# Performance work log

Hardware: AMD Instinct MI355X
Metric: run time of the kernel (lower is better)

Reference implementation:

```python
import jax, jax.numpy as jnp
import numpy as np

B, S, D, H = 4, 2048, 512, 8
HD = D // H


def _xavier(key, shape):
    fan_in, fan_out = shape[1], shape[0]
    limit = float(np.sqrt(6.0 / (fan_in + fan_out)))
    return jax.random.uniform(key, shape, jnp.float32, -limit, limit)


def setup_inputs() -> dict:
    key = jax.random.key(0)
    ks = jax.random.split(key, 7)
    return {
        "query": jax.random.normal(ks[0], (B, S, D), jnp.float32),
        "key": jax.random.normal(ks[1], (B, S, D), jnp.float32),
        "value": jax.random.normal(ks[2], (B, S, D), jnp.float32),
        "Wq": _xavier(ks[3], (D, D)), "bq": jnp.zeros((D,), jnp.float32),
        "Wk": _xavier(ks[4], (D, D)), "bk": jnp.zeros((D,), jnp.float32),
        "Wv": _xavier(ks[5], (D, D)), "bv": jnp.zeros((D,), jnp.float32),
        "Wo": _xavier(ks[6], (D, D)), "bo": jnp.zeros((D,), jnp.float32),
    }


def _split_heads(x):
    # [B,S,D] -> [B,H,S,HD]
    return x.reshape(B, S, H, HD).transpose(0, 2, 1, 3)


def reference(query, key, value, Wq, bq, Wk, bk, Wv, bv, Wo, bo):
    # torch Linear: y = x @ W.T + b
    Q = _split_heads(query @ Wq.T + bq)
    K = _split_heads(key @ Wk.T + bk)
    V = _split_heads(value @ Wv.T + bv)
    scale = 1.0 / jnp.sqrt(jnp.asarray(HD, Q.dtype))
    logits = jnp.einsum("bhqd,bhkd->bhqk", Q, K) * scale  # [B,H,S,S]
    attn = jax.nn.softmax(logits, axis=-1)
    ctx = jnp.einsum("bhqk,bhkd->bhqd", attn, V)
    ctx = ctx.transpose(0, 2, 1, 3).reshape(B, S, D)
    return ctx @ Wo.T + bo
```

## Files before the change

### kernel.cpp

```cpp
#include <hip/hip_runtime.h>
#include <hip/hip_bf16.h>


#define BB 4
#define SS 2048
#define DD 512
#define HH 8
#define HDD 64

typedef __bf16 bf16;
typedef __bf16 bf16x8 __attribute__((ext_vector_type(8)));
typedef float f32x4 __attribute__((ext_vector_type(4)));
typedef float f32x16 __attribute__((ext_vector_type(16)));

__device__ __forceinline__ int swz(int row, int byteInRow) {
    return row * 128 + (byteInRow ^ ((row & 7) << 4));
}

__device__ __forceinline__ void gload16(const void* g, void* l) {
    __builtin_amdgcn_global_load_lds(
        (const __attribute__((address_space(1))) void*)g,
        (__attribute__((address_space(3))) void*)l, 16, 0, 0);
}

__global__ __launch_bounds__(256) void cvt_bf16(
    const float* __restrict__ xq, const float* __restrict__ xk, const float* __restrict__ xv,
    const float* __restrict__ wq, const float* __restrict__ wk, const float* __restrict__ wv,
    const float* __restrict__ wo,
    bf16* __restrict__ xqb, bf16* __restrict__ xkb, bf16* __restrict__ xvb,
    bf16* __restrict__ wqb, bf16* __restrict__ wkb, bf16* __restrict__ wvb,
    bf16* __restrict__ wob)
{
    const int NX = BB * SS * DD / 4;
    const int NW = DD * DD / 4;
    const int total = 3 * NX + 4 * NW;
    for (int g = blockIdx.x * 256 + threadIdx.x; g < total; g += gridDim.x * 256) {
        const float* src; bf16* dst; int off;
        if (g < 3 * NX) {
            int s = g >> 20; off = g & (NX - 1);
            src = s == 0 ? xq : s == 1 ? xk : xv;
            dst = s == 0 ? xqb : s == 1 ? xkb : xvb;
        } else {
            int gg = g - 3 * NX; int s = gg >> 16; off = gg & (NW - 1);
            src = s == 0 ? wq : s == 1 ? wk : s == 2 ? wv : wo;
            dst = s == 0 ? wqb : s == 1 ? wkb : s == 2 ? wvb : wob;
        }
        float4 v = ((const float4*)src)[off];
        union { bf16 h[4]; ushort4 u; } c;
        c.h[0] = (bf16)v.x; c.h[1] = (bf16)v.y; c.h[2] = (bf16)v.z; c.h[3] = (bf16)v.w;
        ((ushort4*)dst)[off] = c.u;
    }
}

__global__ __launch_bounds__(256) void gemm_qkv(
    const bf16* __restrict__ Xq, const bf16* __restrict__ Xk, const bf16* __restrict__ Xv,
    const bf16* __restrict__ Wq, const bf16* __restrict__ Wk, const bf16* __restrict__ Wv,
    const float* __restrict__ bq, const float* __restrict__ bk, const float* __restrict__ bv,
    bf16* __restrict__ Qb, bf16* __restrict__ Kb, bf16* __restrict__ Vt)
{
    const int lin = blockIdx.x;
    const int w = (lin & 7) * 192 + (lin >> 3);
    const int z = w / 512, rem = w & 511;
    const int m0 = (rem >> 3) * 128, n0 = (rem & 7) * 64;

    const bf16* __restrict__ A  = (z == 0) ? Xq : (z == 1) ? Xk : Xv;
    const bf16* __restrict__ Wt = (z == 0) ? Wq : (z == 1) ? Wk : Wv;
    const float* __restrict__ bias = (z == 0) ? bq : (z == 1) ? bk : bv;

    __shared__ char lds[24576];
    char* As = lds;
    char* Bs = lds + 16384;

    const int t = threadIdx.x, wid = t >> 6, lane = t & 63;
    const int lr = lane & 15, lg = lane >> 4;

    float bv4[4];
#pragma unroll
    for (int ni = 0; ni < 4; ni++) bv4[ni] = bias[n0 + ni * 16 + lr];

    const int srow = lane >> 3, s_l = (lane & 7) ^ srow;

    f32x4 acc[2][4] = {};

    for (int k0 = 0; k0 < DD; k0 += 64) {
#pragma unroll
        for (int i = 0; i < 4; i++) {
            int row = 32 * wid + 8 * i + srow;
            gload16(A + (size_t)(m0 + row) * DD + k0 + s_l * 8, As + (32 * wid + 8 * i) * 128);
        }
#pragma unroll
        for (int i = 0; i < 2; i++) {
            int row = 16 * wid + 8 * i + srow;
            gload16(Wt + (size_t)(n0 + row) * DD + k0 + s_l * 8, Bs + (16 * wid + 8 * i) * 128);
        }
        __syncthreads();
#pragma unroll
        for (int kk = 0; kk < 2; kk++) {
            bf16x8 af[2], bfr[4];
#pragma unroll
            for (int mi = 0; mi < 2; mi++)
                af[mi] = *(const bf16x8*)(As + swz(wid * 32 + mi * 16 + lr, kk * 64 + lg * 16));
#pragma unroll
            for (int ni = 0; ni < 4; ni++)
                bfr[ni] = *(const bf16x8*)(Bs + swz(ni * 16 + lr, kk * 64 + lg * 16));
#pragma unroll
            for (int mi = 0; mi < 2; mi++)
#pragma unroll
                for (int ni = 0; ni < 4; ni++)
                    acc[mi][ni] = __builtin_amdgcn_mfma_f32_16x16x32_bf16(af[mi], bfr[ni], acc[mi][ni], 0, 0, 0);
        }
        __syncthreads();
    }

#pragma unroll
    for (int mi = 0; mi < 2; mi++)
#pragma unroll
        for (int ni = 0; ni < 4; ni++) {
            int col = n0 + ni * 16 + lr;
#pragma unroll
            for (int j = 0; j < 4; j++) {
                int row = m0 + wid * 32 + mi * 16 + lg * 4 + j;
                float v = acc[mi][ni][j] + bv4[ni];
                if (z == 0) {
                    Qb[(size_t)row * DD + col] = (bf16)v;
                } else if (z == 1) {
                    Kb[(size_t)row * DD + col] = (bf16)v;
                } else {
                    int b = row >> 11, s = row & 2047, h = col >> 6, d = col & 63;
                    Vt[((((size_t)b * HH + h) * HDD + d) << 11) + s] = (bf16)v;
                }
            }
        }
}

__global__ __launch_bounds__(512) void attn_kernel(
    const bf16* __restrict__ Qb, const bf16* __restrict__ Kb,
    const bf16* __restrict__ Vt, bf16* __restrict__ Ctx)
{
    __shared__ char lds[65536];
    const int t = threadIdx.x, wid = t >> 6, lane = t & 63;
    const int grp = wid >> 2, qw = wid & 3;
    const int l31 = lane & 31, hi = lane >> 5;
    const int lin = blockIdx.x;
    const int wk = (lin & 7) * 64 + (lin >> 3);
    const int qt = wk & 15, bh = wk >> 4;
    const int b = bh >> 3, h = bh & 7;
    const int q0 = qt * 128 + qw * 32;

    const bf16* Qp = Qb + ((size_t)b * SS + q0) * DD + h * HDD;
    const bf16* Kp = Kb + (size_t)b * SS * DD + h * HDD;
    const bf16* Vp = Vt + ((size_t)b * HH + h) * HDD * SS;

    const float qscale = 0.125f * 1.4426950408889634f;
    bf16x8 qf[4];
#pragma unroll
    for (int dk = 0; dk < 4; dk++) {
        bf16x8 v = *(const bf16x8*)(Qp + (size_t)l31 * DD + dk * 16 + hi * 8);
#pragma unroll
        for (int e = 0; e < 8; e++) v[e] = (bf16)((float)v[e] * qscale);
        qf[dk] = v;
    }

    bf16x8 ones;
#pragma unroll
    for (int e = 0; e < 8; e++) ones[e] = (bf16)1.0f;

    const int srow = lane >> 3, s_l = (lane & 7) ^ srow;
    const size_t koff = (size_t)(16 * qw + srow) * DD + s_l * 8;
    const size_t voff = (size_t)(16 * qw + srow) * SS + s_l * 8;

#define STAGE(buf, kvb) do {                                                   \
        char* Kd = lds + grp * 16384 + (buf) * 8192 + qw * 2048;               \
        char* Vd = lds + 32768 + grp * 16384 + (buf) * 8192 + qw * 2048;       \
        gload16(Kp + koff + (size_t)(kvb) * DD, Kd);                           \
        gload16(Kp + koff + 8 * DD + (size_t)(kvb) * DD, Kd + 1024);           \
        gload16(Vp + voff + (kvb), Vd);                                        \
        gload16(Vp + voff + 8 * SS + (kvb), Vd + 1024);                        \
    } while (0)

    STAGE(0, grp * 64);

    f32x16 ctx0 = {}, ctx1 = {}, l4 = {};
    __syncthreads();

    const int NI = SS / 128;
    for (int it = 0; it < NI; ++it) {
        const int cur = it & 1;
        const char* Ks = lds + grp * 16384 + cur * 8192;
        const char* Vs = lds + 32768 + grp * 16384 + cur * 8192;
        if (it + 1 < NI) STAGE(cur ^ 1, (it + 1) * 128 + grp * 64);

        f32x16 p0 = {}, p1 = {};
        __builtin_amdgcn_s_setprio(1);
#pragma unroll
        for (int dk = 0; dk < 4; dk++) {
            bf16x8 kf0 = *(const bf16x8*)(Ks + swz(l31,      dk * 32 + hi * 16));
            bf16x8 kf1 = *(const bf16x8*)(Ks + swz(32 + l31, dk * 32 + hi * 16));
            p0 = __builtin_amdgcn_mfma_f32_32x32x16_bf16(kf0, qf[dk], p0, 0, 0, 0);
            p1 = __builtin_amdgcn_mfma_f32_32x32x16_bf16(kf1, qf[dk], p1, 0, 0, 0);
        }
        __builtin_amdgcn_s_setprio(0);

#pragma unroll
        for (int r = 0; r < 16; r++) {
            p0[r] = __builtin_amdgcn_exp2f(p0[r]);
            p1[r] = __builtin_amdgcn_exp2f(p1[r]);
        }

        __builtin_amdgcn_s_setprio(1);
#define PVBLOCK(P, NTOFF) do {                                                       \
        union { bf16 h[8]; bf16x8 v; } F0, F1;                                       \
        _Pragma("unroll")                                                            \
        for (int e = 0; e < 8; e++) { F0.h[e] = (bf16)P[e]; F1.h[e] = (bf16)P[8 + e]; } \
        l4 = __builtin_amdgcn_mfma_f32_32x32x16_bf16(F0.v, ones, l4, 0, 0, 0);       \
        l4 = __builtin_amdgcn_mfma_f32_32x32x16_bf16(F1.v, ones, l4, 0, 0, 0);       \
        union { ushort4 q[2]; bf16x8 v; } v00, v01, v10, v11;                        \
        v00.q[0] = *(const ushort4*)(Vs + swz(l31,      (NTOFF) + 8 * hi));          \
        v00.q[1] = *(const ushort4*)(Vs + swz(l31,      (NTOFF) + 16 + 8 * hi));     \
        v01.q[0] = *(const ushort4*)(Vs + swz(32 + l31, (NTOFF) + 8 * hi));          \
        v01.q[1] = *(const ushort4*)(Vs + swz(32 + l31, (NTOFF) + 16 + 8 * hi));     \
        v10.q[0] = *(const ushort4*)(Vs + swz(l31,      (NTOFF) + 32 + 8 * hi));     \
        v10.q[1] = *(const ushort4*)(Vs + swz(l31,      (NTOFF) + 48 + 8 * hi));     \
        v11.q[0] = *(const ushort4*)(Vs + swz(32 + l31, (NTOFF) + 32 + 8 * hi));     \
        v11.q[1] = *(const ushort4*)(Vs + swz(32 + l31, (NTOFF) + 48 + 8 * hi));     \
        ctx0 = __builtin_amdgcn_mfma_f32_32x32x16_bf16(F0.v, v00.v, ctx0, 0, 0, 0);  \
        ctx0 = __builtin_amdgcn_mfma_f32_32x32x16_bf16(F1.v, v10.v, ctx0, 0, 0, 0);  \
        ctx1 = __builtin_amdgcn_mfma_f32_32x32x16_bf16(F0.v, v01.v, ctx1, 0, 0, 0);  \
        ctx1 = __builtin_amdgcn_mfma_f32_32x32x16_bf16(F1.v, v11.v, ctx1, 0, 0, 0);  \
    } while (0)

        PVBLOCK(p0, 0);
        PVBLOCK(p1, 64);
#undef PVBLOCK
        __builtin_amdgcn_s_setprio(0);
        __syncthreads();
    }
#undef STAGE

    if (grp == 1) {
        float* dst = (float*)(lds + qw * 12288);
#pragma unroll
        for (int r = 0; r < 16; r++) {
            dst[r * 64 + lane]        = ctx0[r];
            dst[(16 + r) * 64 + lane] = ctx1[r];
            dst[(32 + r) * 64 + lane] = l4[r];
        }
    }
    __syncthreads();
    if (grp == 0) {
        const float* src = (const float*)(lds + qw * 12288);
#pragma unroll
        for (int r = 0; r < 16; r++) {
            ctx0[r] += src[r * 64 + lane];
            ctx1[r] += src[(16 + r) * 64 + lane];
            l4[r]   += src[(32 + r) * 64 + lane];
        }
#pragma unroll
        for (int r = 0; r < 16; r++) {
            int q = (r & 3) + 8 * (r >> 2) + 4 * hi;
            float inv = 1.0f / l4[r];
            size_t base = ((size_t)b * SS + q0 + q) * DD + h * HDD;
            Ctx[base + l31]      = (bf16)(ctx0[r] * inv);
            Ctx[base + 32 + l31] = (bf16)(ctx1[r] * inv);
        }
    }
}

__global__ __launch_bounds__(256) void gemm_out(
    const bf16* __restrict__ A, const bf16* __restrict__ Wt,
    const float* __restrict__ bias, float* __restrict__ Out)
{
    const int lin = blockIdx.x;
    const int w = (lin & 7) * 64 + (lin >> 3);
    const int m0 = (w >> 3) * 128, n0 = (w & 7) * 64;

    __shared__ char lds[24576];
    char* As = lds;
    char* Bs = lds + 16384;

    const int t = threadIdx.x, wid = t >> 6, lane = t & 63;
    const int lr = lane & 15, lg = lane >> 4;

    float bv4[4];
#pragma unroll
    for (int ni = 0; ni < 4; ni++) bv4[ni] = bias[n0 + ni * 16 + lr];

    const int srow = lane >> 3, s_l = (lane & 7) ^ srow;

    f32x4 acc[2][4] = {};

    for (int k0 = 0; k0 < DD; k0 += 64) {
#pragma unroll
        for (int i = 0; i < 4; i++) {
            int row = 32 * wid + 8 * i + srow;
            gload16(A + (size_t)(m0 + row) * DD + k0 + s_l * 8, As + (32 * wid + 8 * i) * 128);
        }
#pragma unroll
        for (int i = 0; i < 2; i++) {
            int row = 16 * wid + 8 * i + srow;
            gload16(Wt + (size_t)(n0 + row) * DD + k0 + s_l * 8, Bs + (16 * wid + 8 * i) * 128);
        }
        __syncthreads();
#pragma unroll
        for (int kk = 0; kk < 2; kk++) {
            bf16x8 af[2], bfr[4];
#pragma unroll
            for (int mi = 0; mi < 2; mi++)
                af[mi] = *(const bf16x8*)(As + swz(wid * 32 + mi * 16 + lr, kk * 64 + lg * 16));
#pragma unroll
            for (int ni = 0; ni < 4; ni++)
                bfr[ni] = *(const bf16x8*)(Bs + swz(ni * 16 + lr, kk * 64 + lg * 16));
#pragma unroll
            for (int mi = 0; mi < 2; mi++)
#pragma unroll
                for (int ni = 0; ni < 4; ni++)
                    acc[mi][ni] = __builtin_amdgcn_mfma_f32_16x16x32_bf16(af[mi], bfr[ni], acc[mi][ni], 0, 0, 0);
        }
        __syncthreads();
    }

#pragma unroll
    for (int mi = 0; mi < 2; mi++)
#pragma unroll
        for (int ni = 0; ni < 4; ni++) {
            int col = n0 + ni * 16 + lr;
#pragma unroll
            for (int j = 0; j < 4; j++) {
                int row = m0 + wid * 32 + mi * 16 + lg * 4 + j;
                Out[(size_t)row * DD + col] = acc[mi][ni][j] + bv4[ni];
            }
        }
}

extern "C" void kernel_launch(void* const* d_in, const int* in_sizes, int n_in,
                              void* d_out, int out_size, void* d_ws, size_t ws_size,
                              hipStream_t stream) {
    (void)in_sizes; (void)n_in; (void)out_size; (void)ws_size;
    const float* q  = (const float*)d_in[0];
    const float* k  = (const float*)d_in[1];
    const float* v  = (const float*)d_in[2];
    const float* Wq = (const float*)d_in[3]; const float* bq = (const float*)d_in[4];
    const float* Wk = (const float*)d_in[5]; const float* bk = (const float*)d_in[6];
    const float* Wv = (const float*)d_in[7]; const float* bv = (const float*)d_in[8];
    const float* Wo = (const float*)d_in[9]; const float* bo = (const float*)d_in[10];
    float* out = (float*)d_out;

    char* ws = (char*)d_ws;
    const size_t MD2 = (size_t)BB * SS * DD * 2;
    const size_t WB  = (size_t)DD * DD * 2;
    bf16* Qb  = (bf16*)(ws);
    bf16* Kb  = (bf16*)(ws + MD2);
    bf16* Vt  = (bf16*)(ws + 2 * MD2);
    bf16* Ctx = (bf16*)(ws + 3 * MD2);
    bf16* Xqb = Ctx;
    bf16* Xkb = (bf16*)(ws + 4 * MD2);
    bf16* Xvb = (bf16*)(ws + 5 * MD2);
    bf16* Wqb = (bf16*)(ws + 6 * MD2);
    bf16* Wkb = (bf16*)(ws + 6 * MD2 + WB);
    bf16* Wvb = (bf16*)(ws + 6 * MD2 + 2 * WB);
    bf16* Wob = (bf16*)(ws + 6 * MD2 + 3 * WB);

    cvt_bf16<<<2048, 256, 0, stream>>>(q, k, v, Wq, Wk, Wv, Wo,
                                       Xqb, Xkb, Xvb, Wqb, Wkb, Wvb, Wob);

    gemm_qkv<<<1536, 256, 0, stream>>>(Xqb, Xkb, Xvb, Wqb, Wkb, Wvb,
                                       bq, bk, bv, Qb, Kb, Vt);

    attn_kernel<<<512, 512, 0, stream>>>(Qb, Kb, Vt, Ctx);

    gemm_out<<<512, 256, 0, stream>>>(Ctx, Wob, bo, out);
}
```

Before: 121.8 us.

## Split attention KV range across separate blocks with a combine kernel

Moves the two-way KV split from two wave groups inside one 512-thread block to separate 256-thread blocks, so 1024 smaller blocks launch instead of 512. Each block writes unnormalized fp16 context partials and fp32 row sums to workspace, and a new combine kernel adds the two halves, normalizes and writes the bf16 context. This removes the in-block LDS reduction and halves LDS per block to allow more flexible scheduling. In exchange it adds global round-trip traffic for the partials, one extra kernel launch, and a risk of fp16 overflow or precision loss in the unnormalized sums.

Measured after the change: 128.8 us. +5.7%, slower.

```diff
diff --git a/kernel.cpp b/kernel.cpp
--- a/kernel.cpp
+++ b/kernel.cpp
@@ -9,6 +9,7 @@
 #define HDD 64
 
 typedef __bf16 bf16;
+typedef _Float16 f16;
 typedef __bf16 bf16x8 __attribute__((ext_vector_type(8)));
 typedef float f32x4 __attribute__((ext_vector_type(4)));
 typedef float f32x16 __attribute__((ext_vector_type(16)));
@@ -133,19 +134,20 @@
         }
 }
 
-__global__ __launch_bounds__(512) void attn_kernel(
+__global__ __launch_bounds__(256) void attn_kernel(
     const bf16* __restrict__ Qb, const bf16* __restrict__ Kb,
-    const bf16* __restrict__ Vt, bf16* __restrict__ Ctx)
-{
-    __shared__ char lds[65536];
+    const bf16* __restrict__ Vt,
+    f16* __restrict__ cp0, f16* __restrict__ cp1, float* __restrict__ lp)
+{
+    __shared__ char lds[32768];
     const int t = threadIdx.x, wid = t >> 6, lane = t & 63;
-    const int grp = wid >> 2, qw = wid & 3;
     const int l31 = lane & 31, hi = lane >> 5;
     const int lin = blockIdx.x;
-    const int wk = (lin & 7) * 64 + (lin >> 3);
-    const int qt = wk & 15, bh = wk >> 4;
+    const int w = (lin & 7) * 128 + (lin >> 3);
+    const int bh = w >> 5, qt = (w >> 1) & 15, kvh = w & 1;
     const int b = bh >> 3, h = bh & 7;
-    const int q0 = qt * 128 + qw * 32;
+    const int q0 = qt * 128 + wid * 32;
+    const int kvbase = kvh * 1024;
 
     const bf16* Qp = Qb + ((size_t)b * SS + q0) * DD + h * HDD;
     const bf16* Kp = Kb + (size_t)b * SS * DD + h * HDD;
@@ -166,29 +168,29 @@
     for (int e = 0; e < 8; e++) ones[e] = (bf16)1.0f;
 
     const int srow = lane >> 3, s_l = (lane & 7) ^ srow;
-    const size_t koff = (size_t)(16 * qw + srow) * DD + s_l * 8;
-    const size_t voff = (size_t)(16 * qw + srow) * SS + s_l * 8;
+    const size_t koff = (size_t)(16 * wid + srow) * DD + s_l * 8;
+    const size_t voff = (size_t)(16 * wid + srow) * SS + s_l * 8;
 
 #define STAGE(buf, kvb) do {                                                   \
-        char* Kd = lds + grp * 16384 + (buf) * 8192 + qw * 2048;               \
-        char* Vd = lds + 32768 + grp * 16384 + (buf) * 8192 + qw * 2048;       \
+        char* Kd = lds + (buf) * 8192 + wid * 2048;                            \
+        char* Vd = lds + 16384 + (buf) * 8192 + wid * 2048;                    \
         gload16(Kp + koff + (size_t)(kvb) * DD, Kd);                           \
         gload16(Kp + koff + 8 * DD + (size_t)(kvb) * DD, Kd + 1024);           \
         gload16(Vp + voff + (kvb), Vd);                                        \
         gload16(Vp + voff + 8 * SS + (kvb), Vd + 1024);                        \
     } while (0)
 
-    STAGE(0, grp * 64);
+    STAGE(0, kvbase);
 
     f32x16 ctx0 = {}, ctx1 = {}, l4 = {};
     __syncthreads();
 
-    const int NI = SS / 128;
+    const int NI = 16;
     for (int it = 0; it < NI; ++it) {
         const int cur = it & 1;
-        const char* Ks = lds + grp * 16384 + cur * 8192;
-        const char* Vs = lds + 32768 + grp * 16384 + cur * 8192;
-        if (it + 1 < NI) STAGE(cur ^ 1, (it + 1) * 128 + grp * 64);
+        const char* Ks = lds + cur * 8192;
+        const char* Vs = lds + 16384 + cur * 8192;
+        if (it + 1 < NI) STAGE(cur ^ 1, kvbase + (it + 1) * 64);
 
         f32x16 p0 = {}, p1 = {};
         __builtin_amdgcn_s_setprio(1);
@@ -237,32 +239,46 @@
     }
 #undef STAGE
 
-    if (grp == 1) {
-        float* dst = (float*)(lds + qw * 12288);
-#pragma unroll
-        for (int r = 0; r < 16; r++) {
-            dst[r * 64 + lane]        = ctx0[r];
-            dst[(16 + r) * 64 + lane] = ctx1[r];
-            dst[(32 + r) * 64 + lane] = l4[r];
-        }
-    }
-    __syncthreads();
-    if (grp == 0) {
-        const float* src = (const float*)(lds + qw * 12288);
-#pragma unroll
-        for (int r = 0; r < 16; r++) {
-            ctx0[r] += src[r * 64 + lane];
-            ctx1[r] += src[(16 + r) * 64 + lane];
-            l4[r]   += src[(32 + r) * 64 + lane];
-        }
-#pragma unroll
-        for (int r = 0; r < 16; r++) {
-            int q = (r & 3) + 8 * (r >> 2) + 4 * hi;
-            float inv = 1.0f / l4[r];
-            size_t base = ((size_t)b * SS + q0 + q) * DD + h * HDD;
-            Ctx[base + l31]      = (bf16)(ctx0[r] * inv);
-            Ctx[base + 32 + l31] = (bf16)(ctx1[r] * inv);
-        }
+    f16* cp = (kvh ? cp1 : cp0) + ((size_t)(bh * 16 + qt)) * 128 * 64;
+    float* lpp = lp + ((size_t)kvh * 512 + bh * 16 + qt) * 128;
+#pragma unroll
+    for (int r = 0; r < 16; r++) {
+        int q = (r & 3) + 8 * (r >> 2) + 4 * hi;
+        int row = wid * 32 + q;
+        cp[row * 64 + l31]      = (f16)ctx0[r];
+        cp[row * 64 + 32 + l31] = (f16)ctx1[r];
+        if (l31 == 0) lpp[row] = l4[r];
+    }
+}
+
+__global__ __launch_bounds__(256) void attn_combine(
+    const f16* __restrict__ cp0, const f16* __restrict__ cp1,
+    const float* __restrict__ lp, bf16* __restrict__ Ctx)
+{
+    const int u = blockIdx.x;
+    const int bh = u >> 4, qt = u & 15;
+    const int b = bh >> 3, h = bh & 7;
+    const int t = threadIdx.x;
+    const int d0 = (t & 7) * 8, r0 = t >> 3;
+
+#pragma unroll
+    for (int rr = 0; rr < 4; rr++) {
+        int row = r0 + rr * 32;
+        float l = lp[(size_t)u * 128 + row] + lp[((size_t)512 + u) * 128 + row];
+        float inv = 1.0f / l;
+        size_t pbase = (size_t)u * 8192 + (size_t)row * 64 + d0;
+        union { uint4 u4; f16 h[8]; } a, c;
+        a.u4 = *(const uint4*)(cp0 + pbase);
+        c.u4 = *(const uint4*)(cp1 + pbase);
+        union { ushort s[8]; uint4 u4; } o;
+#pragma unroll
+        for (int e = 0; e < 8; e++) {
+            union { bf16 b_; ushort us; } cv;
+            cv.b_ = (bf16)(((float)a.h[e] + (float)c.h[e]) * inv);
+            o.s[e] = cv.us;
+        }
+        size_t obase = ((size_t)b * SS + qt * 128 + row) * DD + h * HDD + d0;
+        *(uint4*)(Ctx + obase) = o.u4;
     }
 }
 
@@ -359,6 +375,9 @@
     bf16* Wkb = (bf16*)(ws + 6 * MD2 + WB);
     bf16* Wvb = (bf16*)(ws + 6 * MD2 + 2 * WB);
     bf16* Wob = (bf16*)(ws + 6 * MD2 + 3 * WB);
+    f16*   cp0 = (f16*)(ws + 4 * MD2);
+    f16*   cp1 = (f16*)(ws + 5 * MD2);
+    float* lp  = (float*)(ws + 6 * MD2);
 
     cvt_bf16<<<2048, 256, 0, stream>>>(q, k, v, Wq, Wk, Wv, Wo,
                                        Xqb, Xkb, Xvb, Wqb, Wkb, Wvb, Wob);
@@ -366,7 +385,9 @@
     gemm_qkv<<<1536, 256, 0, stream>>>(Xqb, Xkb, Xvb, Wqb, Wkb, Wvb,
                                        bq, bk, bv, Qb, Kb, Vt);
 
-    attn_kernel<<<512, 512, 0, stream>>>(Qb, Kb, Vt, Ctx);
+    attn_kernel<<<1024, 256, 0, stream>>>(Qb, Kb, Vt, cp0, cp1, lp);
+
+    attn_combine<<<512, 256, 0, stream>>>(cp0, cp1, lp, Ctx);
 
     gemm_out<<<512, 256, 0, stream>>>(Ctx, Wob, bo, out);
 }
```
